# Optimization experiments

Measured on AMD Instinct MI355X. Metric: run time of the kernel, lower is better.

## Reference

```python
import jax, jax.numpy as jnp
import numpy as np

N_NODES = 131072
N_EDGES = 4194304
H1, H2 = 16, 1


def setup_inputs() -> dict:
    key = jax.random.key(0)
    k = jax.random.split(key, 6)
    x = jax.random.uniform(k[0], (N_NODES, 2), dtype=jnp.float32)
    edge_index = jax.random.randint(k[1], (2, N_EDGES), 0, N_NODES, dtype=jnp.int64)
    # GCNConv weights (glorot-ish scale) and zero biases
    W1 = jax.random.normal(k[2], (2, H1), dtype=jnp.float32) * 0.5
    b1 = jnp.zeros((H1,), dtype=jnp.float32)
    W2 = jax.random.normal(k[3], (H1, H2), dtype=jnp.float32) * 0.25
    b2 = jnp.zeros((H2,), dtype=jnp.float32)
    return {"x": x, "W1": W1, "b1": b1, "W2": W2, "b2": b2, "edge_index": edge_index}


def gcn_layer(x, W, b, src, dst, n):
    # PyG GCNConv: h = D^{-1/2} (A+I) D^{-1/2} (x W) + b  (self-loops already in src/dst)
    h = x @ W                                              # [N, F_out]
    deg = jax.ops.segment_sum(jnp.ones(dst.shape[0], h.dtype), dst, num_segments=n)
    dinv = jax.lax.rsqrt(deg)                              # deg >= 1 thanks to self-loops
    norm = dinv[src] * dinv[dst]                           # [E+N]
    out = jax.ops.segment_sum(h[src] * norm[:, None], dst, num_segments=n)
    return out + b


def reference(x, W1, b1, W2, b2, edge_index):
    n = x.shape[0]
    loops = jnp.arange(n, dtype=edge_index.dtype)
    src = jnp.concatenate([edge_index[0], loops])          # add self-loops once
    dst = jnp.concatenate([edge_index[1], loops])
    h = jax.nn.relu(gcn_layer(x, W1, b1, src, dst, n))
    h = gcn_layer(h, W2, b2, src, dst, n)                  # [N, 1]
    scores = jax.nn.sigmoid(h)
    return scores[edge_index[0]]                           # gather per-edge source score [E, 1]
```

## Files before the change

kernel.cpp:

```cpp
#include <hip/hip_runtime.h>
#include <cmath>

typedef unsigned int uint;

constexpr int N  = 131072;
constexpr int E  = 4194304;
constexpr int F  = 16;
constexpr int NB = 512;
constexpr int NBLK  = 512;
constexpr int SCT   = 512;
constexpr int CHUNK = 8192;
constexpr int EPT   = 16;
constexpr int NSCAN = NB * NBLK;
constexpr int CAP   = 10240;

__global__ void k_hist(const int* __restrict__ dst, uint* __restrict__ hist_blocks) {
    __shared__ uint h[NB];
    int t = threadIdx.x, g = blockIdx.x;
    h[t] = 0;
    __syncthreads();
    int base = g * CHUNK;
#pragma unroll
    for (int k = 0; k < EPT; ++k)
        atomicAdd(&h[dst[base + k * SCT + t] >> 8], 1u);
    __syncthreads();
    hist_blocks[(size_t)t * NBLK + g] = h[t];
}

__global__ void k_scan_up(const uint* __restrict__ hist, uint* __restrict__ bsum) {
    __shared__ uint s[256];
    int g = blockIdx.x, t = threadIdx.x;
    s[t] = hist[(size_t)g * 256 + t];
    __syncthreads();
    for (int off = 128; off > 0; off >>= 1) {
        if (t < off) s[t] += s[t + off];
        __syncthreads();
    }
    if (t == 0) bsum[g] = s[0];
}

__global__ void k_scan_mid(uint* bsum) {
    __shared__ uint s[256];
    int t = threadIdx.x;
    uint v[4]; uint sum = 0;
#pragma unroll
    for (int k = 0; k < 4; ++k) { v[k] = bsum[t * 4 + k]; sum += v[k]; }
    s[t] = sum;
    __syncthreads();
    for (int off = 1; off < 256; off <<= 1) {
        uint x = (t >= off) ? s[t - off] : 0u;
        __syncthreads();
        s[t] += x;
        __syncthreads();
    }
    uint base = (t == 0) ? 0u : s[t - 1];
#pragma unroll
    for (int k = 0; k < 4; ++k) { uint old = v[k]; bsum[t * 4 + k] = base; base += old; }
}

__global__ void k_scan_down(const uint* __restrict__ hist, const uint* __restrict__ bsum,
                            uint* __restrict__ scanned) {
    __shared__ uint s[256];
    int g = blockIdx.x, t = threadIdx.x;
    uint v = hist[(size_t)g * 256 + t];
    s[t] = v;
    __syncthreads();
    for (int off = 1; off < 256; off <<= 1) {
        uint x = (t >= off) ? s[t - off] : 0u;
        __syncthreads();
        s[t] += x;
        __syncthreads();
    }
    scanned[(size_t)g * 256 + t] = bsum[g] + s[t] - v;
}

__global__ void __launch_bounds__(SCT) k_scatter(
        const int* __restrict__ src, const int* __restrict__ dst,
        const uint* __restrict__ scanned, uint* __restrict__ part) {
    __shared__ uint h[NB];
    __shared__ uint sc[NB];
    __shared__ uint wb[NB];
    __shared__ uint vals[CHUNK];
    __shared__ uint addr[CHUNK];
    int t = threadIdx.x, g = blockIdx.x;
    h[t] = 0;
    __syncthreads();
    int d[EPT], s[EPT];
    int base = g * CHUNK;
#pragma unroll
    for (int k = 0; k < EPT; ++k) {
        int e = base + k * SCT + t;
        d[k] = dst[e];
        s[k] = src[e];
        atomicAdd(&h[d[k] >> 8], 1u);
    }
    __syncthreads();
    uint v = h[t];
    sc[t] = v;
    __syncthreads();
    for (int off = 1; off < NB; off <<= 1) {
        uint x = (t >= off) ? sc[t - off] : 0u;
        __syncthreads();
        sc[t] += x;
        __syncthreads();
    }
    uint ex = sc[t] - v;
    wb[t] = scanned[(size_t)t * NBLK + g] - ex;
    h[t] = ex;
    __syncthreads();
#pragma unroll
    for (int k = 0; k < EPT; ++k) {
        int b = d[k] >> 8;
        uint slot = atomicAdd(&h[b], 1u);
        vals[slot] = ((uint)s[k] << 8) | (uint)(d[k] & 255);
        addr[slot] = wb[b] + slot;
    }
    __syncthreads();
#pragma unroll
    for (int k = 0; k < EPT; ++k) {
        int i = k * SCT + t;
        part[addr[i]] = vals[i];
    }
}

__global__ void __launch_bounds__(SCT) k_sort(
        uint* part, const uint* __restrict__ scanned,
        const float* __restrict__ x,
        uint* __restrict__ csr, float* __restrict__ dinv, float2* __restrict__ y) {
    __shared__ uint cnt[256];
    __shared__ uint sc[256];
    __shared__ uint bump[256];
    __shared__ uint srt[CAP];
    int t = threadIdx.x, b = blockIdx.x;
    if (t < 256) cnt[t] = 0;
    __syncthreads();
    uint S0 = scanned[(size_t)b * NBLK];
    uint S1 = (b == NB - 1) ? (uint)E : scanned[(size_t)(b + 1) * NBLK];
    for (uint i = S0 + t; i < S1; i += SCT) atomicAdd(&cnt[part[i] & 255u], 1u);
    __syncthreads();
    if (t < 256) sc[t] = cnt[t];
    __syncthreads();
    for (int off = 1; off < 256; off <<= 1) {
        uint xx = 0;
        if (t < 256 && t >= off) xx = sc[t - off];
        __syncthreads();
        if (t < 256) sc[t] += xx;
        __syncthreads();
    }
    if (t < 256) bump[t] = sc[t] - cnt[t];
    __syncthreads();
    for (uint i = S0 + t; i < S1; i += SCT) {
        uint pk = part[i];
        uint slot = atomicAdd(&bump[pk & 255u], 1u);
        srt[slot] = pk >> 8;
    }
    __syncthreads();
    uint L = S1 - S0;
    for (uint i = t; i < L; i += SCT) part[S0 + i] = srt[i];
    if (t < 256) {
        int node = (b << 8) + t;
        uint ex = sc[t] - cnt[t];
        csr[node] = S0 + ex;
        float di = rsqrtf(1.0f + (float)cnt[t]);
        dinv[node] = di;
        float2 xv = ((const float2*)x)[node];
        y[node] = make_float2(di * xv.x, di * xv.y);
    }
}

__global__ void k_l1(const uint* __restrict__ srcs, const uint* __restrict__ csr,
                     const float2* __restrict__ y, const float* __restrict__ dinv,
                     const float* __restrict__ W1, const float* __restrict__ b1,
                     const float* __restrict__ W2, float* __restrict__ g2) {
    int tid = blockIdx.x * blockDim.x + threadIdx.x;
    int node = tid >> 2, lane = tid & 3;
    uint o0 = csr[node];
    uint o1 = (node == N - 1) ? (uint)E : csr[node + 1];
    float A0 = 0.0f, A1 = 0.0f;
    for (uint j = o0 + lane; j < o1; j += 4) {
        float2 ys = y[srcs[j]];
        A0 += ys.x; A1 += ys.y;
    }
    A0 += __shfl_xor(A0, 1); A0 += __shfl_xor(A0, 2);
    A1 += __shfl_xor(A1, 1); A1 += __shfl_xor(A1, 2);
    float di = dinv[node];
    float2 yn = y[node];
    A0 = di * (A0 + yn.x);
    A1 = di * (A1 + yn.y);
    float acc = 0.0f;
#pragma unroll
    for (int f = lane; f < F; f += 4) {
        float v = fmaf(A0, W1[f], fmaf(A1, W1[F + f], b1[f]));
        acc = fmaf(fmaxf(v, 0.0f), W2[f], acc);
    }
    acc += __shfl_xor(acc, 1); acc += __shfl_xor(acc, 2);
    if (lane == 0) g2[node] = di * acc;
}

__global__ void k_l2(const uint* __restrict__ srcs, const uint* __restrict__ csr,
                     const float* __restrict__ g2, const float* __restrict__ dinv,
                     const float* __restrict__ b2, float* __restrict__ scores) {
    int tid = blockIdx.x * blockDim.x + threadIdx.x;
    int node = tid >> 2, lane = tid & 3;
    uint o0 = csr[node];
    uint o1 = (node == N - 1) ? (uint)E : csr[node + 1];
    float acc = 0.0f;
    for (uint j = o0 + lane; j < o1; j += 4) acc += g2[srcs[j]];
    acc += __shfl_xor(acc, 1); acc += __shfl_xor(acc, 2);
    if (lane == 0) {
        float v = fmaf(dinv[node], acc + g2[node], b2[0]);
        scores[node] = 1.0f / (1.0f + expf(-v));
    }
}

__global__ void k_out(const int* __restrict__ src, const float* __restrict__ scores,
                      float* __restrict__ out) {
    int e = blockIdx.x * blockDim.x + threadIdx.x;
    if (e < E) out[e] = scores[src[e]];
}

extern "C" void kernel_launch(void* const* d_in, const int* in_sizes, int n_in,
                              void* d_out, int out_size, void* d_ws, size_t ws_size,
                              hipStream_t stream) {
    const float* x  = (const float*)d_in[0];
    const float* W1 = (const float*)d_in[1];
    const float* b1 = (const float*)d_in[2];
    const float* W2 = (const float*)d_in[3];
    const float* b2 = (const float*)d_in[4];
    const int*   ei = (const int*)d_in[5];
    const int* src = ei;
    const int* dst = ei + E;

    uint* hist_blocks = (uint*)d_ws;
    uint* scanned     = hist_blocks + NSCAN;
    uint* bsum        = scanned + NSCAN;
    uint* csr         = bsum + 1024;
    float* dinv       = (float*)(csr + N + 2);
    float2* y         = (float2*)(dinv + N);
    float* g2         = (float*)(y + N);
    float* scores     = g2 + N;

    uint* part  = (uint*)d_out;
    float* out  = (float*)d_out;

    k_hist     <<<NBLK,        SCT, 0, stream>>>(dst, hist_blocks);
    k_scan_up  <<<NSCAN / 256, 256, 0, stream>>>(hist_blocks, bsum);
    k_scan_mid <<<1,           256, 0, stream>>>(bsum);
    k_scan_down<<<NSCAN / 256, 256, 0, stream>>>(hist_blocks, bsum, scanned);
    k_scatter  <<<NBLK,        SCT, 0, stream>>>(src, dst, scanned, part);
    k_sort     <<<NB,          SCT, 0, stream>>>(part, scanned, x, csr, dinv, y);
    k_l1       <<<(N * 4) / 256, 256, 0, stream>>>(part, csr, y, dinv, W1, b1, W2, g2);
    k_l2       <<<(N * 4) / 256, 256, 0, stream>>>(part, csr, g2, dinv, b2, scores);
    k_out      <<<E / 256,     256, 0, stream>>>(src, scores, out);
}
```

Baseline: 195.9 us.

## Use per-wave LDS histograms, shuffle scans, and eight lanes per node

New measurement: 191.3 us. -2.3%, faster.

```diff
diff --git a/kernel.cpp b/kernel.cpp
--- a/kernel.cpp
+++ b/kernel.cpp
@@ -13,18 +13,26 @@
 constexpr int EPT   = 16;
 constexpr int NSCAN = NB * NBLK;
 constexpr int CAP   = 10240;
-
-__global__ void k_hist(const int* __restrict__ dst, uint* __restrict__ hist_blocks) {
-    __shared__ uint h[NB];
+constexpr int SLOTS = CAP / SCT;
+constexpr int LPN   = 8;
+
+__global__ void __launch_bounds__(SCT) k_hist(const int* __restrict__ dst,
+                                              uint* __restrict__ hist_blocks) {
+    __shared__ uint hw[8 * NB];
     int t = threadIdx.x, g = blockIdx.x;
-    h[t] = 0;
+    int w = t >> 6;
+#pragma unroll
+    for (int k = 0; k < 8; ++k) hw[k * SCT + t] = 0;
     __syncthreads();
     int base = g * CHUNK;
 #pragma unroll
     for (int k = 0; k < EPT; ++k)
-        atomicAdd(&h[dst[base + k * SCT + t] >> 8], 1u);
-    __syncthreads();
-    hist_blocks[(size_t)t * NBLK + g] = h[t];
+        atomicAdd(&hw[w * NB + (dst[base + k * SCT + t] >> 8)], 1u);
+    __syncthreads();
+    uint sum = 0;
+#pragma unroll
+    for (int k = 0; k < 8; ++k) sum += hw[k * NB + t];
+    hist_blocks[(size_t)t * NBLK + g] = sum;
 }
 
 __global__ void k_scan_up(const uint* __restrict__ hist, uint* __restrict__ bsum) {
@@ -78,11 +86,12 @@
         const int* __restrict__ src, const int* __restrict__ dst,
         const uint* __restrict__ scanned, uint* __restrict__ part) {
     __shared__ uint h[NB];
-    __shared__ uint sc[NB];
     __shared__ uint wb[NB];
+    __shared__ uint wsum[8];
     __shared__ uint vals[CHUNK];
     __shared__ uint addr[CHUNK];
     int t = threadIdx.x, g = blockIdx.x;
+    int lane = t & 63, w = t >> 6;
     h[t] = 0;
     __syncthreads();
     int d[EPT], s[EPT];
@@ -96,15 +105,18 @@
     }
     __syncthreads();
     uint v = h[t];
-    sc[t] = v;
-    __syncthreads();
-    for (int off = 1; off < NB; off <<= 1) {
-        uint x = (t >= off) ? sc[t - off] : 0u;
-        __syncthreads();
-        sc[t] += x;
-        __syncthreads();
-    }
-    uint ex = sc[t] - v;
+    uint sv = v;
+#pragma unroll
+    for (int off = 1; off < 64; off <<= 1) {
+        uint n = __shfl_up(sv, off);
+        if (lane >= off) sv += n;
+    }
+    if (lane == 63) wsum[w] = sv;
+    __syncthreads();
+    uint wo = 0;
+    for (int i = 0; i < w; ++i) wo += wsum[i];
+    sv += wo;
+    uint ex = sv - v;
     wb[t] = scanned[(size_t)t * NBLK + g] - ex;
     h[t] = ex;
     __syncthreads();
@@ -127,40 +139,65 @@
         uint* part, const uint* __restrict__ scanned,
         const float* __restrict__ x,
         uint* __restrict__ csr, float* __restrict__ dinv, float2* __restrict__ y) {
+    __shared__ uint hw[8 * 256];
     __shared__ uint cnt[256];
     __shared__ uint sc[256];
-    __shared__ uint bump[256];
+    __shared__ uint wsum[4];
     __shared__ uint srt[CAP];
     int t = threadIdx.x, b = blockIdx.x;
-    if (t < 256) cnt[t] = 0;
+    int lane = t & 63, w = t >> 6;
+#pragma unroll
+    for (int k = 0; k < 4; ++k) hw[k * SCT + t] = 0;
     __syncthreads();
     uint S0 = scanned[(size_t)b * NBLK];
     uint S1 = (b == NB - 1) ? (uint)E : scanned[(size_t)(b + 1) * NBLK];
-    for (uint i = S0 + t; i < S1; i += SCT) atomicAdd(&cnt[part[i] & 255u], 1u);
-    __syncthreads();
-    if (t < 256) sc[t] = cnt[t];
-    __syncthreads();
-    for (int off = 1; off < 256; off <<= 1) {
-        uint xx = 0;
-        if (t < 256 && t >= off) xx = sc[t - off];
-        __syncthreads();
-        if (t < 256) sc[t] += xx;
-        __syncthreads();
-    }
-    if (t < 256) bump[t] = sc[t] - cnt[t];
-    __syncthreads();
-    for (uint i = S0 + t; i < S1; i += SCT) {
-        uint pk = part[i];
-        uint slot = atomicAdd(&bump[pk & 255u], 1u);
-        srt[slot] = pk >> 8;
+    uint pk[SLOTS];
+#pragma unroll
+    for (int k = 0; k < SLOTS; ++k) {
+        uint i = S0 + (uint)(k * SCT + t);
+        pk[k] = (i < S1) ? part[i] : 0xFFFFFFFFu;
+        if (pk[k] != 0xFFFFFFFFu) atomicAdd(&hw[w * 256 + (pk[k] & 255u)], 1u);
+    }
+    __syncthreads();
+    if (t < 256) {
+        uint tot = 0;
+#pragma unroll
+        for (int k = 0; k < 8; ++k) {
+            uint c = hw[k * 256 + t];
+            hw[k * 256 + t] = tot;
+            tot += c;
+        }
+        cnt[t] = tot;
+        uint sv = tot;
+#pragma unroll
+        for (int off = 1; off < 64; off <<= 1) {
+            uint n = __shfl_up(sv, off);
+            if (lane >= off) sv += n;
+        }
+        if (lane == 63) wsum[t >> 6] = sv;
+        sc[t] = sv;
+    }
+    __syncthreads();
+    if (t < 256) {
+        uint wo = 0;
+        for (int i = 0; i < (t >> 6); ++i) wo += wsum[i];
+        sc[t] += wo;
+    }
+    __syncthreads();
+#pragma unroll
+    for (int k = 0; k < SLOTS; ++k) {
+        if (pk[k] != 0xFFFFFFFFu) {
+            uint bin = pk[k] & 255u;
+            uint slot = (sc[bin] - cnt[bin]) + atomicAdd(&hw[w * 256 + bin], 1u);
+            srt[slot] = pk[k] >> 8;
+        }
     }
     __syncthreads();
     uint L = S1 - S0;
     for (uint i = t; i < L; i += SCT) part[S0 + i] = srt[i];
     if (t < 256) {
         int node = (b << 8) + t;
-        uint ex = sc[t] - cnt[t];
-        csr[node] = S0 + ex;
+        csr[node] = S0 + (sc[t] - cnt[t]);
         float di = rsqrtf(1.0f + (float)cnt[t]);
         dinv[node] = di;
         float2 xv = ((const float2*)x)[node];
@@ -173,27 +210,27 @@
                      const float* __restrict__ W1, const float* __restrict__ b1,
                      const float* __restrict__ W2, float* __restrict__ g2) {
     int tid = blockIdx.x * blockDim.x + threadIdx.x;
-    int node = tid >> 2, lane = tid & 3;
+    int node = tid >> 3, lane = tid & (LPN - 1);
     uint o0 = csr[node];
     uint o1 = (node == N - 1) ? (uint)E : csr[node + 1];
     float A0 = 0.0f, A1 = 0.0f;
-    for (uint j = o0 + lane; j < o1; j += 4) {
+    for (uint j = o0 + lane; j < o1; j += LPN) {
         float2 ys = y[srcs[j]];
         A0 += ys.x; A1 += ys.y;
     }
-    A0 += __shfl_xor(A0, 1); A0 += __shfl_xor(A0, 2);
-    A1 += __shfl_xor(A1, 1); A1 += __shfl_xor(A1, 2);
+    A0 += __shfl_xor(A0, 1); A0 += __shfl_xor(A0, 2); A0 += __shfl_xor(A0, 4);
+    A1 += __shfl_xor(A1, 1); A1 += __shfl_xor(A1, 2); A1 += __shfl_xor(A1, 4);
     float di = dinv[node];
     float2 yn = y[node];
     A0 = di * (A0 + yn.x);
     A1 = di * (A1 + yn.y);
     float acc = 0.0f;
 #pragma unroll
-    for (int f = lane; f < F; f += 4) {
+    for (int f = lane; f < F; f += LPN) {
         float v = fmaf(A0, W1[f], fmaf(A1, W1[F + f], b1[f]));
         acc = fmaf(fmaxf(v, 0.0f), W2[f], acc);
     }
-    acc += __shfl_xor(acc, 1); acc += __shfl_xor(acc, 2);
+    acc += __shfl_xor(acc, 1); acc += __shfl_xor(acc, 2); acc += __shfl_xor(acc, 4);
     if (lane == 0) g2[node] = di * acc;
 }
 
@@ -201,12 +238,12 @@
                      const float* __restrict__ g2, const float* __restrict__ dinv,
                      const float* __restrict__ b2, float* __restrict__ scores) {
     int tid = blockIdx.x * blockDim.x + threadIdx.x;
-    int node = tid >> 2, lane = tid & 3;
+    int node = tid >> 3, lane = tid & (LPN - 1);
     uint o0 = csr[node];
     uint o1 = (node == N - 1) ? (uint)E : csr[node + 1];
     float acc = 0.0f;
-    for (uint j = o0 + lane; j < o1; j += 4) acc += g2[srcs[j]];
-    acc += __shfl_xor(acc, 1); acc += __shfl_xor(acc, 2);
+    for (uint j = o0 + lane; j < o1; j += LPN) acc += g2[srcs[j]];
+    acc += __shfl_xor(acc, 1); acc += __shfl_xor(acc, 2); acc += __shfl_xor(acc, 4);
     if (lane == 0) {
         float v = fmaf(dinv[node], acc + g2[node], b2[0]);
         scores[node] = 1.0f / (1.0f + expf(-v));
@@ -243,13 +280,13 @@
     uint* part  = (uint*)d_out;
     float* out  = (float*)d_out;
 
-    k_hist     <<<NBLK,        SCT, 0, stream>>>(dst, hist_blocks);
-    k_scan_up  <<<NSCAN / 256, 256, 0, stream>>>(hist_blocks, bsum);
-    k_scan_mid <<<1,           256, 0, stream>>>(bsum);
-    k_scan_down<<<NSCAN / 256, 256, 0, stream>>>(hist_blocks, bsum, scanned);
-    k_scatter  <<<NBLK,        SCT, 0, stream>>>(src, dst, scanned, part);
-    k_sort     <<<NB,          SCT, 0, stream>>>(part, scanned, x, csr, dinv, y);
-    k_l1       <<<(N * 4) / 256, 256, 0, stream>>>(part, csr, y, dinv, W1, b1, W2, g2);
-    k_l2       <<<(N * 4) / 256, 256, 0, stream>>>(part, csr, g2, dinv, b2, scores);
-    k_out      <<<E / 256,     256, 0, stream>>>(src, scores, out);
-}
+    k_hist     <<<NBLK,          SCT, 0, stream>>>(dst, hist_blocks);
+    k_scan_up  <<<NSCAN / 256,   256, 0, stream>>>(hist_blocks, bsum);
+    k_scan_mid <<<1,             256, 0, stream>>>(bsum);
+    k_scan_down<<<NSCAN / 256,   256, 0, stream>>>(hist_blocks, bsum, scanned);
+    k_scatter  <<<NBLK,          SCT, 0, stream>>>(src, dst, scanned, part);
+    k_sort     <<<NB,            SCT, 0, stream>>>(part, scanned, x, csr, dinv, y);
+    k_l1       <<<(N * LPN) / 256, 256, 0, stream>>>(part, csr, y, dinv, W1, b1, W2, g2);
+    k_l2       <<<(N * LPN) / 256, 256, 0, stream>>>(part, csr, g2, dinv, b2, scores);
+    k_out      <<<E / 256,       256, 0, stream>>>(src, scores, out);
+}
```
